# Kernel tuning notes

Measured on AMD Instinct MI355X. Metric: run time of the kernel, lower is better.

## Reference

```python
import jax, jax.numpy as jnp
import numpy as np

N_AGENTS, N_ENEMIES, N_ACTIONS = 8, 8, 14
ALLY_F, ENEMY_F = 8, 6
EMBED, RNN, HYPEMB, HYPHID = 32, 64, 64, 64
STATE_DIM = N_AGENTS * ALLY_F + N_ENEMIES * ENEMY_F + N_AGENTS * N_ACTIONS  # 224


def setup_inputs() -> dict:
    key = jax.random.key(0)
    ks = jax.random.split(key, 16)
    b, t = 64, 256
    rn = lambda k, s, sc=0.05: jax.random.normal(k, s, jnp.float32) * sc
    return dict(
        qvals=rn(ks[0], (b, t, N_AGENTS), 1.0),
        states=rn(ks[1], (b, t, STATE_DIM), 1.0),
        hidden_states=rn(ks[2], (b, t, N_AGENTS, RNN), 1.0),
        hw1_w=rn(ks[3], (RNN, EMBED)), hw1_b=jnp.zeros((EMBED,), jnp.float32),
        en_h1w=rn(ks[4], (ENEMY_F, HYPHID)), en_h1b=jnp.zeros((HYPHID,), jnp.float32),
        en_h2w=rn(ks[5], (HYPHID, ENEMY_F * HYPEMB)), en_h2b=jnp.zeros((ENEMY_F * HYPEMB,), jnp.float32),
        en_bias=jnp.zeros((1, HYPEMB), jnp.float32),
        al_h1w=rn(ks[6], (ALLY_F, HYPHID)), al_h1b=jnp.zeros((HYPHID,), jnp.float32),
        al_h2w=rn(ks[7], (HYPHID, ALLY_F * HYPEMB)), al_h2b=jnp.zeros((ALLY_F * HYPEMB,), jnp.float32),
        al_bias=jnp.zeros((1, HYPEMB), jnp.float32),
        act_w=rn(ks[8], (N_ACTIONS, HYPEMB)), act_b=jnp.zeros((HYPEMB,), jnp.float32),
        hb1_w=rn(ks[9], (HYPEMB, EMBED)), hb1_b=jnp.zeros((EMBED,), jnp.float32),
        hw2_w=rn(ks[10], (HYPEMB, EMBED)), hw2_b=jnp.zeros((EMBED,), jnp.float32),
        hb2_w=rn(ks[11], (HYPEMB, 1)), hb2_b=jnp.zeros((1,), jnp.float32),
    )


def _hyperlinear(x, h1w, h1b, h2w, h2b, bias, din, dout):
    # hypernet MLP -> per-sample weight matrix [rows, din, dout]
    h = jax.nn.relu(x @ h1w + h1b)
    W = (h @ h2w + h2b).reshape(-1, din, dout)
    return jnp.einsum('bi,bio->bo', x, W) + bias


def reference(qvals, states, hidden_states, hw1_w, hw1_b,
              en_h1w, en_h1b, en_h2w, en_h2b, en_bias,
              al_h1w, al_h1b, al_h2w, al_h2b, al_bias,
              act_w, act_b, hb1_w, hb1_b, hw2_w, hw2_b, hb2_w, hb2_b):
    b, t, _ = qvals.shape
    BT = b * t
    s = states.reshape(BT, STATE_DIM)
    ally = s[:, :N_AGENTS * ALLY_F].reshape(-1, ALLY_F)                # [BT*A, 8]
    enemy = s[:, N_AGENTS * ALLY_F:N_AGENTS * ALLY_F + N_ENEMIES * ENEMY_F].reshape(-1, ENEMY_F)
    actions = s[:, N_AGENTS * ALLY_F + N_ENEMIES * ENEMY_F:].reshape(BT, N_AGENTS, N_ACTIONS)

    embed_ally = _hyperlinear(ally, al_h1w, al_h1b, al_h2w, al_h2b, al_bias,
                              ALLY_F, HYPEMB).reshape(BT, N_AGENTS, HYPEMB).mean(axis=1)
    embed_enemy = _hyperlinear(enemy, en_h1w, en_h1b, en_h2w, en_h2b, en_bias,
                               ENEMY_F, HYPEMB).reshape(BT, N_ENEMIES, HYPEMB).mean(axis=1)
    embed_action = (actions @ act_w + act_b).mean(axis=1)
    se = jax.nn.relu(embed_ally + embed_enemy + embed_action)          # [BT, HYPEMB]

    w1 = jax.nn.softmax((hidden_states @ hw1_w + hw1_b).reshape(BT, N_AGENTS, EMBED), axis=1)
    b1 = (se @ hb1_w + hb1_b).reshape(BT, 1, EMBED)
    w2 = jnp.abs(se @ hw2_w + hw2_b).reshape(BT, EMBED, 1)
    b2 = (se @ hb2_w + hb2_b).reshape(BT, 1, 1)

    q = qvals.reshape(BT, 1, N_AGENTS)
    hidden = jax.nn.elu(jnp.matmul(q, w1) + b1)                        # [BT, 1, EMBED]
    y = jnp.matmul(hidden, w2) + b2                                    # [BT, 1, 1]
    return y.reshape(b, t, 1)
```

## Files before the change

### kernel.cpp

```cpp
#include <hip/hip_runtime.h>
#include <hip/hip_bf16.h>
#include <stdint.h>

typedef unsigned short u16t;
typedef float f32x4 __attribute__((ext_vector_type(4)));
typedef short bf16x8 __attribute__((ext_vector_type(8)));

#define SDIM 224

__device__ __forceinline__ float lo16(uint32_t w) { union { uint32_t u; float f; } v; v.u = w << 16; return v.f; }
__device__ __forceinline__ float hi16(uint32_t w) { union { uint32_t u; float f; } v; v.u = w & 0xFFFF0000u; return v.f; }
__device__ __forceinline__ uint32_t f2bf(float f) {
    union { float f; uint32_t u; } v; v.f = f;
    return (v.u + 0x7FFFu + ((v.u >> 16) & 1u)) >> 16;
}

__global__ void prep_wt_kernel(const float* __restrict__ h2wA, const float* __restrict__ h2wB,
                               const float* __restrict__ h2bA, const float* __restrict__ h2bB,
                               const float* __restrict__ actw,
                               const float* __restrict__ hb1w, const float* __restrict__ hw2w,
                               const float* __restrict__ hw1w,
                               u16t* __restrict__ wtA, u16t* __restrict__ wtB,
                               u16t* __restrict__ wt2, u16t* __restrict__ wtM)
{
    const int t0 = blockIdx.x * 256 + threadIdx.x, stride = gridDim.x * 256;
    for (int e = t0; e < 34816; e += stride) {
        int j = e & 7, n = (e >> 3) & 63, kb = e >> 9;
        int k = kb * 8 + j;
        float v = 0.f;
        if (k < 512)      { int h = k & 63, i = k >> 6; v = h2wA[h * 512 + i * 64 + n]; }
        else if (k < 520) v = h2bA[(k - 512) * 64 + n];
        wtA[e] = (u16t)f2bf(v);
    }
    for (int e = t0; e < 26624; e += stride) {
        int j = e & 7, n = (e >> 3) & 63, kb = e >> 9;
        int k = kb * 8 + j;
        float v = 0.f;
        if (k < 384)      { int h = k & 63, i = k >> 6; v = h2wB[h * 384 + i * 64 + n]; }
        else if (k < 390) v = h2bB[(k - 384) * 64 + n];
        else if (k < 404) v = actw[(k - 390) * 64 + n];
        wtB[e] = (u16t)f2bf(v);
    }
    for (int e = t0; e < 4096; e += stride) {
        int j = e & 7, n = (e >> 3) & 63, kb = e >> 9;
        int k = kb * 8 + j;
        float v = (n < 32) ? hb1w[k * 32 + n] : hw2w[k * 32 + (n - 32)];
        wt2[e] = (u16t)f2bf(v);
    }
    for (int e = t0; e < 2048; e += stride) {
        int j = e & 7, n = (e >> 3) & 31, kb = e >> 8;
        wtM[e] = (u16t)f2bf(hw1w[(kb * 8 + j) * 32 + n]);
    }
}

template<int DIN, int KP, int FOFF>
__device__ __forceinline__ void stage1(const u16t (*xb)[SDIM], u16t* __restrict__ ps,
                                       const float* __restrict__ s_h1w, float b1r,
                                       int wave, int lane)
{
    float w1r[DIN];
#pragma unroll
    for (int i = 0; i < DIN; ++i) w1r[i] = s_h1w[i * 64 + lane];
#pragma unroll 1
    for (int ss = 0; ss < 2; ++ss) {
        const int s = wave * 2 + ss;
        const u16t* xr = &xb[s][FOFF];
        float psv[DIN];
#pragma unroll
        for (int i = 0; i < DIN; ++i) psv[i] = 0.f;
#pragma unroll
        for (int a = 0; a < 8; ++a) {
            float x[DIN];
            if constexpr (DIN == 8) {
                uint4 v = *(const uint4*)(xr + a * 8);
                x[0] = lo16(v.x); x[1] = hi16(v.x); x[2] = lo16(v.y); x[3] = hi16(v.y);
                x[4] = lo16(v.z); x[5] = hi16(v.z); x[6] = lo16(v.w); x[7] = hi16(v.w);
            } else {
                uint32_t w0 = *(const uint32_t*)(xr + a * 6);
                uint32_t w1 = *(const uint32_t*)(xr + a * 6 + 2);
                uint32_t w2 = *(const uint32_t*)(xr + a * 6 + 4);
                x[0] = lo16(w0); x[1] = hi16(w0); x[2] = lo16(w1);
                x[3] = hi16(w1); x[4] = lo16(w2); x[5] = hi16(w2);
            }
            float hacc = b1r;
#pragma unroll
            for (int i = 0; i < DIN; ++i) hacc += x[i] * w1r[i];
            hacc = fmaxf(hacc, 0.f);
#pragma unroll
            for (int i = 0; i < DIN; ++i) psv[i] += hacc * x[i];
        }
#pragma unroll
        for (int i = 0; i < DIN; ++i) ps[s * KP + i * 64 + lane] = (u16t)f2bf(psv[i]);
    }
}

__global__ __launch_bounds__(256, 7)
void fused_mixer(const float* __restrict__ qvals, const float* __restrict__ states,
                 const float* __restrict__ hs,
                 const float* __restrict__ al_h1w, const float* __restrict__ al_h1b,
                 const float* __restrict__ en_h1w, const float* __restrict__ en_h1b,
                 const float* __restrict__ al_bias, const float* __restrict__ en_bias,
                 const float* __restrict__ act_b,
                 const float* __restrict__ hb1_b, const float* __restrict__ hw2_b,
                 const float* __restrict__ hw1_b, const float* __restrict__ hb2_w,
                 const float* __restrict__ hb2_b,
                 const u16t* __restrict__ wtA, const u16t* __restrict__ wtB,
                 const u16t* __restrict__ wt2, const u16t* __restrict__ wtM,
                 float* __restrict__ out)
{
    constexpr int KPA = 552, KPB = 424;
    __shared__ __align__(16) char s_un[9216];
    __shared__ __align__(16) u16t s_xb[8][SDIM];
    __shared__ __align__(16) u16t s_se[8 * 72];
    __shared__ float s_b1w2[8][64];
    __shared__ float s_b2[8];
    __shared__ float s_q[64];
    __shared__ float s_h1wA[512], s_h1wB[384];
    __shared__ float s_h1bA[64], s_h1bB[64], s_bias3[64], s_hb2w[64];
    __shared__ float s_b1b[32], s_w2b[32], s_w1b[32];
    __shared__ float s_hb2bv;

    const int tid  = threadIdx.x;
    const int wave = tid >> 6;
    const int lane = tid & 63;
    const int lr = lane & 15, lg = lane >> 4;
    const int sbase = blockIdx.x * 8;
    const int o = wave * 16 + lr;

    for (int i = tid; i < 8 * 28; i += 256) {
        int s = i / 28, c = i - s * 28;
        const float4* sp = (const float4*)(states + (size_t)(sbase + s) * SDIM + c * 8);
        float4 v0 = sp[0], v1 = sp[1];
        uint4 p;
        p.x = f2bf(v0.x) | (f2bf(v0.y) << 16);
        p.y = f2bf(v0.z) | (f2bf(v0.w) << 16);
        p.z = f2bf(v1.x) | (f2bf(v1.y) << 16);
        p.w = f2bf(v1.z) | (f2bf(v1.w) << 16);
        *(uint4*)&s_xb[s][c * 8] = p;
    }
    for (int i = tid; i < 512; i += 256) s_h1wA[i] = al_h1w[i];
    for (int i = tid; i < 384; i += 256) s_h1wB[i] = en_h1w[i];
    if (tid < 64) {
        s_h1bA[tid] = al_h1b[tid]; s_h1bB[tid] = en_h1b[tid];
        s_bias3[tid] = al_bias[tid] + en_bias[tid] + act_b[tid];
        s_hb2w[tid] = hb2_w[tid];
        s_q[tid] = qvals[(size_t)sbase * 8 + tid];
    }
    if (tid >= 64 && tid < 96)   s_b1b[tid - 64] = hb1_b[tid - 64];
    if (tid >= 96 && tid < 128)  s_w2b[tid - 96] = hw2_b[tid - 96];
    if (tid >= 128 && tid < 160) s_w1b[tid - 128] = hw1_b[tid - 128];
    if (tid == 160) s_hb2bv = hb2_b[0];
    __syncthreads();

    u16t* ps = (u16t*)s_un;

    stage1<8, KPA, 0>(s_xb, ps, s_h1wA, s_h1bA[lane], wave, lane);
    if (tid < 64) {
        int s = tid >> 3, i = tid & 7;
        float t = 0.f;
#pragma unroll
        for (int a = 0; a < 8; ++a) t += lo16((uint32_t)s_xb[s][a * 8 + i]);
        ps[s * KPA + 512 + i] = (u16t)f2bf(t);
    } else if (tid < 160) {
        int idx = tid - 64;
        int s = idx / 12, kp = idx - s * 12;
        *(uint32_t*)&ps[s * KPA + 520 + kp * 2] = 0u;
    }
    __syncthreads();

    f32x4 accA = {0.f, 0.f, 0.f, 0.f};
    {
        const u16t* arow = ps + (lr & 7) * KPA + lg * 8;
        const bf16x8* wt8 = (const bf16x8*)wtA;
#pragma unroll 4
        for (int kk = 0; kk < 544; kk += 32) {
            bf16x8 av = *(const bf16x8*)(arow + kk);
            bf16x8 bv = wt8[((kk >> 3) + lg) * 64 + o];
            accA = __builtin_amdgcn_mfma_f32_16x16x32_bf16(av, bv, accA, 0, 0, 0);
        }
    }
    __syncthreads();

    float4 hsr[4];
    {
        const float4* hsv = (const float4*)(hs + (size_t)sbase * 512);
#pragma unroll
        for (int i = 0; i < 4; ++i) hsr[i] = hsv[i * 256 + tid];
    }

    stage1<6, KPB, 64>(s_xb, ps, s_h1wB, s_h1bB[lane], wave, lane);
    if (tid < 48) {
        int s = tid / 6, i = tid - s * 6;
        float t = 0.f;
#pragma unroll
        for (int a = 0; a < 8; ++a) t += lo16((uint32_t)s_xb[s][64 + a * 6 + i]);
        ps[s * KPB + 384 + i] = (u16t)f2bf(t);
    } else if (tid >= 64 && tid < 176) {
        int idx = tid - 64;
        int s = idx / 14, j = idx - s * 14;
        float t = 0.f;
#pragma unroll
        for (int a = 0; a < 8; ++a) t += lo16((uint32_t)s_xb[s][112 + a * 14 + j]);
        ps[s * KPB + 390 + j] = (u16t)f2bf(t);
    } else if (tid >= 192 && tid < 240) {
        int idx = tid - 192;
        int s = idx / 6, kp = idx - s * 6;
        *(uint32_t*)&ps[s * KPB + 404 + kp * 2] = 0u;
    }
    __syncthreads();

    {
        f32x4 accB = {0.f, 0.f, 0.f, 0.f};
        const u16t* arow = ps + (lr & 7) * KPB + lg * 8;
        const bf16x8* wt8 = (const bf16x8*)wtB;
#pragma unroll 4
        for (int kk = 0; kk < 416; kk += 32) {
            bf16x8 av = *(const bf16x8*)(arow + kk);
            bf16x8 bv = wt8[((kk >> 3) + lg) * 64 + o];
            accB = __builtin_amdgcn_mfma_f32_16x16x32_bf16(av, bv, accB, 0, 0, 0);
        }
        if (lg < 2) {
#pragma unroll
            for (int j = 0; j < 4; ++j) {
                const int row = lg * 4 + j;
                float se = (accA[j] + accB[j]) * 0.125f + s_bias3[o];
                s_se[row * 72 + o] = (u16t)f2bf(fmaxf(se, 0.f));
            }
        }
    }
    __syncthreads();

    u16t* s_hs = (u16t*)s_un;
    {
#pragma unroll
        for (int i = 0; i < 4; ++i) {
            const int idx = i * 256 + tid;
            const int row = idx >> 4, c4 = idx & 15;
            uint2 p;
            p.x = f2bf(hsr[i].x) | (f2bf(hsr[i].y) << 16);
            p.y = f2bf(hsr[i].z) | (f2bf(hsr[i].w) << 16);
            *(uint2*)&s_hs[row * 72 + c4 * 4] = p;
        }
    }
    {
        f32x4 acc = {0.f, 0.f, 0.f, 0.f};
        const u16t* serow = &s_se[(lr & 7) * 72 + lg * 8];
        const bf16x8* wt8 = (const bf16x8*)wt2;
#pragma unroll
        for (int ks = 0; ks < 2; ++ks) {
            bf16x8 av = *(const bf16x8*)(serow + ks * 32);
            bf16x8 bv = wt8[(ks * 4 + lg) * 64 + o];
            acc = __builtin_amdgcn_mfma_f32_16x16x32_bf16(av, bv, acc, 0, 0, 0);
        }
        if (lg < 2) {
#pragma unroll
            for (int j = 0; j < 4; ++j) {
                const int row = lg * 4 + j;
                float v = acc[j] + ((o < 32) ? s_b1b[o] : s_w2b[o - 32]);
                if (o >= 32) v = fabsf(v);
                s_b1w2[row][o] = v;
            }
        }
    }
    {
        const int smp = wave * 2 + (lg & 1);
        float p = 0.f;
#pragma unroll
        for (int c = 0; c < 4; ++c) {
            const int oo = c * 16 + lr;
            p += lo16((uint32_t)s_se[smp * 72 + oo]) * s_hb2w[oo];
        }
        p += __shfl_xor(p, 1); p += __shfl_xor(p, 2);
        p += __shfl_xor(p, 4); p += __shfl_xor(p, 8);
        if (lr == 0 && lg < 2) s_b2[smp] = p + s_hb2bv;
    }
    __syncthreads();

    bf16x8 bfr[2][2];
    {
        const bf16x8* wtm8 = (const bf16x8*)wtM;
#pragma unroll
        for (int n = 0; n < 2; ++n)
#pragma unroll
            for (int ks = 0; ks < 2; ++ks)
                bfr[n][ks] = wtm8[(ks * 4 + lg) * 32 + n * 16 + lr];
    }
    {
        const float zb0 = s_w1b[lr], zb1 = s_w1b[16 + lr];
        f32x4 d0 = {0.f,0.f,0.f,0.f}, d1 = {0.f,0.f,0.f,0.f};
#pragma unroll
        for (int ks = 0; ks < 2; ++ks) {
            bf16x8 av = *(const bf16x8*)&s_hs[(wave * 16 + lr) * 72 + ks * 32 + lg * 8];
            d0 = __builtin_amdgcn_mfma_f32_16x16x32_bf16(av, bfr[0][ks], d0, 0, 0, 0);
            d1 = __builtin_amdgcn_mfma_f32_16x16x32_bf16(av, bfr[1][ks], d1, 0, 0, 0);
        }
        const int sloc = wave * 2 + (lg >> 1);
        float z0[4], z1[4];
#pragma unroll
        for (int j = 0; j < 4; ++j) { z0[j] = d0[j] + zb0; z1[j] = d1[j] + zb1; }
        float m0 = fmaxf(fmaxf(z0[0], z0[1]), fmaxf(z0[2], z0[3]));
        float m1 = fmaxf(fmaxf(z1[0], z1[1]), fmaxf(z1[2], z1[3]));
        m0 = fmaxf(m0, __shfl_xor(m0, 16));
        m1 = fmaxf(m1, __shfl_xor(m1, 16));
        float qa[4];
        {
            float4 qv = *(const float4*)&s_q[sloc * 8 + (lg & 1) * 4];
            qa[0] = qv.x; qa[1] = qv.y; qa[2] = qv.z; qa[3] = qv.w;
        }
        float s0 = 0.f, s1 = 0.f, hp0 = 0.f, hp1 = 0.f;
#pragma unroll
        for (int j = 0; j < 4; ++j) {
            float e0 = __expf(z0[j] - m0), e1 = __expf(z1[j] - m1);
            s0 += e0; s1 += e1;
            hp0 += qa[j] * e0; hp1 += qa[j] * e1;
        }
        s0  += __shfl_xor(s0, 16);  s1  += __shfl_xor(s1, 16);
        hp0 += __shfl_xor(hp0, 16); hp1 += __shfl_xor(hp1, 16);

        const float b1_0 = s_b1w2[sloc][lr],      b1_1 = s_b1w2[sloc][16 + lr];
        const float w2_0 = s_b1w2[sloc][32 + lr], w2_1 = s_b1w2[sloc][48 + lr];
        float h0 = hp0 / s0 + b1_0; h0 = (h0 > 0.f) ? h0 : (__expf(h0) - 1.f);
        float h1 = hp1 / s1 + b1_1; h1 = (h1 > 0.f) ? h1 : (__expf(h1) - 1.f);
        float yp = h0 * w2_0 + h1 * w2_1;
        yp += __shfl_xor(yp, 1); yp += __shfl_xor(yp, 2);
        yp += __shfl_xor(yp, 4); yp += __shfl_xor(yp, 8);
        if (lr == 0 && (lg & 1) == 0) out[sbase + sloc] = yp + s_b2[sloc];
    }
}

extern "C" void kernel_launch(void* const* d_in, const int* in_sizes, int n_in,
                              void* d_out, int out_size, void* d_ws, size_t ws_size,
                              hipStream_t stream) {
    const float* qvals   = (const float*)d_in[0];
    const float* states  = (const float*)d_in[1];
    const float* hstates = (const float*)d_in[2];
    const float* hw1_w   = (const float*)d_in[3];
    const float* hw1_b   = (const float*)d_in[4];
    const float* en_h1w  = (const float*)d_in[5];
    const float* en_h1b  = (const float*)d_in[6];
    const float* en_h2w  = (const float*)d_in[7];
    const float* en_h2b  = (const float*)d_in[8];
    const float* en_bias = (const float*)d_in[9];
    const float* al_h1w  = (const float*)d_in[10];
    const float* al_h1b  = (const float*)d_in[11];
    const float* al_h2w  = (const float*)d_in[12];
    const float* al_h2b  = (const float*)d_in[13];
    const float* al_bias = (const float*)d_in[14];
    const float* act_w   = (const float*)d_in[15];
    const float* act_b   = (const float*)d_in[16];
    const float* hb1_w   = (const float*)d_in[17];
    const float* hb1_b   = (const float*)d_in[18];
    const float* hw2_w   = (const float*)d_in[19];
    const float* hw2_b   = (const float*)d_in[20];
    const float* hb2_w   = (const float*)d_in[21];
    const float* hb2_b   = (const float*)d_in[22];

    u16t* wtA = (u16t*)d_ws;
    u16t* wtB = wtA + 34816;
    u16t* wt2 = wtA + 61440;
    u16t* wtM = wtA + 65536;

    prep_wt_kernel<<<64, 256, 0, stream>>>(al_h2w, en_h2w, al_h2b, en_h2b, act_w,
                                           hb1_w, hw2_w, hw1_w, wtA, wtB, wt2, wtM);
    fused_mixer<<<2048, 256, 0, stream>>>(qvals, states, hstates,
                                          al_h1w, al_h1b, en_h1w, en_h1b,
                                          al_bias, en_bias, act_b,
                                          hb1_b, hw2_b, hw1_b, hb2_w, hb2_b,
                                          wtA, wtB, wt2, wtM, (float*)d_out);
}
```

Measured before the change: 38.17 us.

## Merge ally/enemy hypernet GEMMs into one K=960 pass and reorder mixing stage

Concatenates the ally and enemy/action weight panels into one workspace matrix. Both stage-1 passes now write into a single wide shared buffer, so one MFMA loop over K=960 replaces two GEMMs and removes two block barriers. The hidden-state tile is staged to shared memory up front, and the softmax mixing MFMA now runs before the main GEMM. qvals are read directly from global memory. The larger shared footprint and the lowered launch-bounds target (7 to 4 blocks per SM) may reduce occupancy.

After: 36.34 us. 4.8% less time.

```diff
diff --git a/kernel.cpp b/kernel.cpp
--- a/kernel.cpp
+++ b/kernel.cpp
@@ -20,26 +20,23 @@
                                const float* __restrict__ actw,
                                const float* __restrict__ hb1w, const float* __restrict__ hw2w,
                                const float* __restrict__ hw1w,
-                               u16t* __restrict__ wtA, u16t* __restrict__ wtB,
-                               u16t* __restrict__ wt2, u16t* __restrict__ wtM)
+                               u16t* __restrict__ wtAB, u16t* __restrict__ wt2,
+                               u16t* __restrict__ wtM)
 {
     const int t0 = blockIdx.x * 256 + threadIdx.x, stride = gridDim.x * 256;
-    for (int e = t0; e < 34816; e += stride) {
+    for (int e = t0; e < 61440; e += stride) {
         int j = e & 7, n = (e >> 3) & 63, kb = e >> 9;
         int k = kb * 8 + j;
         float v = 0.f;
         if (k < 512)      { int h = k & 63, i = k >> 6; v = h2wA[h * 512 + i * 64 + n]; }
         else if (k < 520) v = h2bA[(k - 512) * 64 + n];
-        wtA[e] = (u16t)f2bf(v);
-    }
-    for (int e = t0; e < 26624; e += stride) {
-        int j = e & 7, n = (e >> 3) & 63, kb = e >> 9;
-        int k = kb * 8 + j;
-        float v = 0.f;
-        if (k < 384)      { int h = k & 63, i = k >> 6; v = h2wB[h * 384 + i * 64 + n]; }
-        else if (k < 390) v = h2bB[(k - 384) * 64 + n];
-        else if (k < 404) v = actw[(k - 390) * 64 + n];
-        wtB[e] = (u16t)f2bf(v);
+        else if (k >= 544) {
+            int k2 = k - 544;
+            if (k2 < 384)      { int h = k2 & 63, i = k2 >> 6; v = h2wB[h * 384 + i * 64 + n]; }
+            else if (k2 < 390) v = h2bB[(k2 - 384) * 64 + n];
+            else if (k2 < 404) v = actw[(k2 - 390) * 64 + n];
+        }
+        wtAB[e] = (u16t)f2bf(v);
     }
     for (int e = t0; e < 4096; e += stride) {
         int j = e & 7, n = (e >> 3) & 63, kb = e >> 9;
@@ -94,7 +91,7 @@
     }
 }
 
-__global__ __launch_bounds__(256, 7)
+__global__ __launch_bounds__(256, 4)
 void fused_mixer(const float* __restrict__ qvals, const float* __restrict__ states,
                  const float* __restrict__ hs,
                  const float* __restrict__ al_h1w, const float* __restrict__ al_h1b,
@@ -104,17 +101,17 @@
                  const float* __restrict__ hb1_b, const float* __restrict__ hw2_b,
                  const float* __restrict__ hw1_b, const float* __restrict__ hb2_w,
                  const float* __restrict__ hb2_b,
-                 const u16t* __restrict__ wtA, const u16t* __restrict__ wtB,
-                 const u16t* __restrict__ wt2, const u16t* __restrict__ wtM,
+                 const u16t* __restrict__ wtAB, const u16t* __restrict__ wt2,
+                 const u16t* __restrict__ wtM,
                  float* __restrict__ out)
 {
-    constexpr int KPA = 552, KPB = 424;
-    __shared__ __align__(16) char s_un[9216];
+    constexpr int KP = 968;
+    __shared__ __align__(16) u16t s_ps[8 * KP];
+    __shared__ __align__(16) u16t s_hs[64 * 72];
     __shared__ __align__(16) u16t s_xb[8][SDIM];
     __shared__ __align__(16) u16t s_se[8 * 72];
     __shared__ float s_b1w2[8][64];
     __shared__ float s_b2[8];
-    __shared__ float s_q[64];
     __shared__ float s_h1wA[512], s_h1wB[384];
     __shared__ float s_h1bA[64], s_h1bB[64], s_bias3[64], s_hb2w[64];
     __shared__ float s_b1b[32], s_w2b[32], s_w1b[32];
@@ -138,13 +135,25 @@
         p.w = f2bf(v1.z) | (f2bf(v1.w) << 16);
         *(uint4*)&s_xb[s][c * 8] = p;
     }
+    {
+        const float4* hsv = (const float4*)(hs + (size_t)sbase * 512);
+#pragma unroll
+        for (int i = 0; i < 4; ++i) {
+            const int idx = i * 256 + tid;
+            float4 v = hsv[idx];
+            const int row = idx >> 4, c4 = idx & 15;
+            uint2 p;
+            p.x = f2bf(v.x) | (f2bf(v.y) << 16);
+            p.y = f2bf(v.z) | (f2bf(v.w) << 16);
+            *(uint2*)&s_hs[row * 72 + c4 * 4] = p;
+        }
+    }
     for (int i = tid; i < 512; i += 256) s_h1wA[i] = al_h1w[i];
     for (int i = tid; i < 384; i += 256) s_h1wB[i] = en_h1w[i];
     if (tid < 64) {
         s_h1bA[tid] = al_h1b[tid]; s_h1bB[tid] = en_h1b[tid];
         s_bias3[tid] = al_bias[tid] + en_bias[tid] + act_b[tid];
         s_hb2w[tid] = hb2_w[tid];
-        s_q[tid] = qvals[(size_t)sbase * 8 + tid];
     }
     if (tid >= 64 && tid < 96)   s_b1b[tid - 64] = hb1_b[tid - 64];
     if (tid >= 96 && tid < 128)  s_w2b[tid - 96] = hw2_b[tid - 96];
@@ -152,141 +161,50 @@
     if (tid == 160) s_hb2bv = hb2_b[0];
     __syncthreads();
 
-    u16t* ps = (u16t*)s_un;
-
-    stage1<8, KPA, 0>(s_xb, ps, s_h1wA, s_h1bA[lane], wave, lane);
+    stage1<8, KP, 0>(s_xb, s_ps, s_h1wA, s_h1bA[lane], wave, lane);
+    stage1<6, KP, 64>(s_xb, s_ps + 544, s_h1wB, s_h1bB[lane], wave, lane);
     if (tid < 64) {
         int s = tid >> 3, i = tid & 7;
         float t = 0.f;
 #pragma unroll
         for (int a = 0; a < 8; ++a) t += lo16((uint32_t)s_xb[s][a * 8 + i]);
-        ps[s * KPA + 512 + i] = (u16t)f2bf(t);
-    } else if (tid < 160) {
+        s_ps[s * KP + 512 + i] = (u16t)f2bf(t);
+    } else if (tid < 112) {
         int idx = tid - 64;
-        int s = idx / 12, kp = idx - s * 12;
-        *(uint32_t*)&ps[s * KPA + 520 + kp * 2] = 0u;
-    }
-    __syncthreads();
-
-    f32x4 accA = {0.f, 0.f, 0.f, 0.f};
-    {
-        const u16t* arow = ps + (lr & 7) * KPA + lg * 8;
-        const bf16x8* wt8 = (const bf16x8*)wtA;
-#pragma unroll 4
-        for (int kk = 0; kk < 544; kk += 32) {
-            bf16x8 av = *(const bf16x8*)(arow + kk);
-            bf16x8 bv = wt8[((kk >> 3) + lg) * 64 + o];
-            accA = __builtin_amdgcn_mfma_f32_16x16x32_bf16(av, bv, accA, 0, 0, 0);
-        }
-    }
-    __syncthreads();
-
-    float4 hsr[4];
-    {
-        const float4* hsv = (const float4*)(hs + (size_t)sbase * 512);
-#pragma unroll
-        for (int i = 0; i < 4; ++i) hsr[i] = hsv[i * 256 + tid];
-    }
-
-    stage1<6, KPB, 64>(s_xb, ps, s_h1wB, s_h1bB[lane], wave, lane);
-    if (tid < 48) {
-        int s = tid / 6, i = tid - s * 6;
+        int s = idx / 6, i = idx - s * 6;
         float t = 0.f;
 #pragma unroll
         for (int a = 0; a < 8; ++a) t += lo16((uint32_t)s_xb[s][64 + a * 6 + i]);
-        ps[s * KPB + 384 + i] = (u16t)f2bf(t);
-    } else if (tid >= 64 && tid < 176) {
-        int idx = tid - 64;
+        s_ps[s * KP + 928 + i] = (u16t)f2bf(t);
+    } else if (tid < 224) {
+        int idx = tid - 112;
         int s = idx / 14, j = idx - s * 14;
         float t = 0.f;
 #pragma unroll
         for (int a = 0; a < 8; ++a) t += lo16((uint32_t)s_xb[s][112 + a * 14 + j]);
-        ps[s * KPB + 390 + j] = (u16t)f2bf(t);
-    } else if (tid >= 192 && tid < 240) {
-        int idx = tid - 192;
-        int s = idx / 6, kp = idx - s * 6;
-        *(uint32_t*)&ps[s * KPB + 404 + kp * 2] = 0u;
-    }
-    __syncthreads();
-
-    {
-        f32x4 accB = {0.f, 0.f, 0.f, 0.f};
-        const u16t* arow = ps + (lr & 7) * KPB + lg * 8;
-        const bf16x8* wt8 = (const bf16x8*)wtB;
-#pragma unroll 4
-        for (int kk = 0; kk < 416; kk += 32) {
-            bf16x8 av = *(const bf16x8*)(arow + kk);
-            bf16x8 bv = wt8[((kk >> 3) + lg) * 64 + o];
-            accB = __builtin_amdgcn_mfma_f32_16x16x32_bf16(av, bv, accB, 0, 0, 0);
-        }
-        if (lg < 2) {
-#pragma unroll
-            for (int j = 0; j < 4; ++j) {
-                const int row = lg * 4 + j;
-                float se = (accA[j] + accB[j]) * 0.125f + s_bias3[o];
-                s_se[row * 72 + o] = (u16t)f2bf(fmaxf(se, 0.f));
-            }
-        }
-    }
-    __syncthreads();
-
-    u16t* s_hs = (u16t*)s_un;
-    {
-#pragma unroll
-        for (int i = 0; i < 4; ++i) {
-            const int idx = i * 256 + tid;
-            const int row = idx >> 4, c4 = idx & 15;
-            uint2 p;
-            p.x = f2bf(hsr[i].x) | (f2bf(hsr[i].y) << 16);
-            p.y = f2bf(hsr[i].z) | (f2bf(hsr[i].w) << 16);
-            *(uint2*)&s_hs[row * 72 + c4 * 4] = p;
-        }
-    }
-    {
-        f32x4 acc = {0.f, 0.f, 0.f, 0.f};
-        const u16t* serow = &s_se[(lr & 7) * 72 + lg * 8];
-        const bf16x8* wt8 = (const bf16x8*)wt2;
-#pragma unroll
-        for (int ks = 0; ks < 2; ++ks) {
-            bf16x8 av = *(const bf16x8*)(serow + ks * 32);
-            bf16x8 bv = wt8[(ks * 4 + lg) * 64 + o];
-            acc = __builtin_amdgcn_mfma_f32_16x16x32_bf16(av, bv, acc, 0, 0, 0);
-        }
-        if (lg < 2) {
-#pragma unroll
-            for (int j = 0; j < 4; ++j) {
-                const int row = lg * 4 + j;
-                float v = acc[j] + ((o < 32) ? s_b1b[o] : s_w2b[o - 32]);
-                if (o >= 32) v = fabsf(v);
-                s_b1w2[row][o] = v;
-            }
-        }
-    }
-    {
-        const int smp = wave * 2 + (lg & 1);
-        float p = 0.f;
-#pragma unroll
-        for (int c = 0; c < 4; ++c) {
-            const int oo = c * 16 + lr;
-            p += lo16((uint32_t)s_se[smp * 72 + oo]) * s_hb2w[oo];
-        }
-        p += __shfl_xor(p, 1); p += __shfl_xor(p, 2);
-        p += __shfl_xor(p, 4); p += __shfl_xor(p, 8);
-        if (lr == 0 && lg < 2) s_b2[smp] = p + s_hb2bv;
-    }
-    __syncthreads();
-
-    bf16x8 bfr[2][2];
-    {
+        s_ps[s * KP + 934 + j] = (u16t)f2bf(t);
+    } else {
+        int idx = tid - 224;
+        int s = idx >> 2, c = idx & 3;
+#pragma unroll
+        for (int u = 0; u < 3; ++u)
+            *(uint32_t*)&s_ps[s * KP + 520 + c * 6 + u * 2] = 0u;
+        if (c < 3)
+            *(uint32_t*)&s_ps[s * KP + 948 + c * 4] = 0u;
+        else
+            *(uint32_t*)&s_ps[s * KP + 948 + 8 + 2] = 0u;
+    }
+
+    float hp0, hp1, s0, s1;
+    {
+        bf16x8 bfr[2][2];
         const bf16x8* wtm8 = (const bf16x8*)wtM;
 #pragma unroll
         for (int n = 0; n < 2; ++n)
 #pragma unroll
             for (int ks = 0; ks < 2; ++ks)
                 bfr[n][ks] = wtm8[(ks * 4 + lg) * 32 + n * 16 + lr];
-    }
-    {
-        const float zb0 = s_w1b[lr], zb1 = s_w1b[16 + lr];
+
         f32x4 d0 = {0.f,0.f,0.f,0.f}, d1 = {0.f,0.f,0.f,0.f};
 #pragma unroll
         for (int ks = 0; ks < 2; ++ks) {
@@ -295,6 +213,7 @@
             d1 = __builtin_amdgcn_mfma_f32_16x16x32_bf16(av, bfr[1][ks], d1, 0, 0, 0);
         }
         const int sloc = wave * 2 + (lg >> 1);
+        const float zb0 = s_w1b[lr], zb1 = s_w1b[16 + lr];
         float z0[4], z1[4];
 #pragma unroll
         for (int j = 0; j < 4; ++j) { z0[j] = d0[j] + zb0; z1[j] = d1[j] + zb1; }
@@ -304,10 +223,11 @@
         m1 = fmaxf(m1, __shfl_xor(m1, 16));
         float qa[4];
         {
-            float4 qv = *(const float4*)&s_q[sloc * 8 + (lg & 1) * 4];
+            const float* qp = qvals + (size_t)(sbase + sloc) * 8 + (lg & 1) * 4;
+            float4 qv = *(const float4*)qp;
             qa[0] = qv.x; qa[1] = qv.y; qa[2] = qv.z; qa[3] = qv.w;
         }
-        float s0 = 0.f, s1 = 0.f, hp0 = 0.f, hp1 = 0.f;
+        s0 = 0.f; s1 = 0.f; hp0 = 0.f; hp1 = 0.f;
 #pragma unroll
         for (int j = 0; j < 4; ++j) {
             float e0 = __expf(z0[j] - m0), e1 = __expf(z1[j] - m1);
@@ -316,7 +236,66 @@
         }
         s0  += __shfl_xor(s0, 16);  s1  += __shfl_xor(s1, 16);
         hp0 += __shfl_xor(hp0, 16); hp1 += __shfl_xor(hp1, 16);
-
+    }
+    __syncthreads();
+
+    {
+        f32x4 acc = {0.f, 0.f, 0.f, 0.f};
+        const u16t* arow = s_ps + (lr & 7) * KP + lg * 8;
+        const bf16x8* wt8 = (const bf16x8*)wtAB;
+#pragma unroll 5
+        for (int kk = 0; kk < 960; kk += 32) {
+            bf16x8 av = *(const bf16x8*)(arow + kk);
+            bf16x8 bv = wt8[((kk >> 3) + lg) * 64 + o];
+            acc = __builtin_amdgcn_mfma_f32_16x16x32_bf16(av, bv, acc, 0, 0, 0);
+        }
+        if (lg < 2) {
+#pragma unroll
+            for (int j = 0; j < 4; ++j) {
+                const int row = lg * 4 + j;
+                float se = acc[j] * 0.125f + s_bias3[o];
+                s_se[row * 72 + o] = (u16t)f2bf(fmaxf(se, 0.f));
+            }
+        }
+    }
+    __syncthreads();
+
+    {
+        f32x4 acc = {0.f, 0.f, 0.f, 0.f};
+        const u16t* serow = &s_se[(lr & 7) * 72 + lg * 8];
+        const bf16x8* wt8 = (const bf16x8*)wt2;
+#pragma unroll
+        for (int ks = 0; ks < 2; ++ks) {
+            bf16x8 av = *(const bf16x8*)(serow + ks * 32);
+            bf16x8 bv = wt8[(ks * 4 + lg) * 64 + o];
+            acc = __builtin_amdgcn_mfma_f32_16x16x32_bf16(av, bv, acc, 0, 0, 0);
+        }
+        if (lg < 2) {
+#pragma unroll
+            for (int j = 0; j < 4; ++j) {
+                const int row = lg * 4 + j;
+                float v = acc[j] + ((o < 32) ? s_b1b[o] : s_w2b[o - 32]);
+                if (o >= 32) v = fabsf(v);
+                s_b1w2[row][o] = v;
+            }
+        }
+    }
+    {
+        const int smp = wave * 2 + (lg & 1);
+        float p = 0.f;
+#pragma unroll
+        for (int c = 0; c < 4; ++c) {
+            const int oo = c * 16 + lr;
+            p += lo16((uint32_t)s_se[smp * 72 + oo]) * s_hb2w[oo];
+        }
+        p += __shfl_xor(p, 1); p += __shfl_xor(p, 2);
+        p += __shfl_xor(p, 4); p += __shfl_xor(p, 8);
+        if (lr == 0 && lg < 2) s_b2[smp] = p + s_hb2bv;
+    }
+    __syncthreads();
+
+    {
+        const int sloc = wave * 2 + (lg >> 1);
         const float b1_0 = s_b1w2[sloc][lr],      b1_1 = s_b1w2[sloc][16 + lr];
         const float w2_0 = s_b1w2[sloc][32 + lr], w2_1 = s_b1w2[sloc][48 + lr];
         float h0 = hp0 / s0 + b1_0; h0 = (h0 > 0.f) ? h0 : (__expf(h0) - 1.f);
@@ -355,16 +334,15 @@
     const float* hb2_w   = (const float*)d_in[21];
     const float* hb2_b   = (const float*)d_in[22];
 
-    u16t* wtA = (u16t*)d_ws;
-    u16t* wtB = wtA + 34816;
-    u16t* wt2 = wtA + 61440;
-    u16t* wtM = wtA + 65536;
+    u16t* wtAB = (u16t*)d_ws;
+    u16t* wt2  = wtAB + 61440;
+    u16t* wtM  = wtAB + 65536;
 
     prep_wt_kernel<<<64, 256, 0, stream>>>(al_h2w, en_h2w, al_h2b, en_h2b, act_w,
-                                           hb1_w, hw2_w, hw1_w, wtA, wtB, wt2, wtM);
+                                           hb1_w, hw2_w, hw1_w, wtAB, wt2, wtM);
     fused_mixer<<<2048, 256, 0, stream>>>(qvals, states, hstates,
                                           al_h1w, al_h1b, en_h1w, en_h1b,
                                           al_bias, en_bias, act_b,
                                           hb1_b, hw2_b, hw1_b, hb2_w, hb2_b,
-                                          wtA, wtB, wt2, wtM, (float*)d_out);
-}
+                                          wtAB, wt2, wtM, (float*)d_out);
+}
```

## Process 16 samples per block to fill MFMA rows and keep states in fp32

Applied to the files above, without the earlier changes.

Each block now handles 16 samples instead of 8, so the 16-row MFMA tiles are fully used rather than half wasted, and the grid is halved. The states tile is kept in shared memory as fp32 instead of being converted to bf16, and the action sums are computed directly from global memory. Bf16 conversion now goes through the HIP intrinsics, with a packed two-value variant. Shared memory and register use roughly double and the launch bound drops to 4 blocks per CU, which lowers occupancy.

Result: faster. 34.81 us (-8.8%).

```diff
diff --git a/kernel.cpp b/kernel.cpp
--- a/kernel.cpp
+++ b/kernel.cpp
@@ -9,10 +9,13 @@
 #define SDIM 224
 
 __device__ __forceinline__ float lo16(uint32_t w) { union { uint32_t u; float f; } v; v.u = w << 16; return v.f; }
-__device__ __forceinline__ float hi16(uint32_t w) { union { uint32_t u; float f; } v; v.u = w & 0xFFFF0000u; return v.f; }
-__device__ __forceinline__ uint32_t f2bf(float f) {
-    union { float f; uint32_t u; } v; v.f = f;
-    return (v.u + 0x7FFFu + ((v.u >> 16) & 1u)) >> 16;
+__device__ __forceinline__ u16t bf1(float a) {
+    union { __hip_bfloat16 h; u16t u; } c; c.h = __float2bfloat16(a); return c.u;
+}
+__device__ __forceinline__ uint32_t pk2(float a, float b) {
+    union { __hip_bfloat162 h; uint32_t u; } c;
+    c.h = __float22bfloat162_rn(make_float2(a, b));
+    return c.u;
 }
 
 __global__ void prep_wt_kernel(const float* __restrict__ h2wA, const float* __restrict__ h2wB,
@@ -30,7 +33,7 @@
         float v = 0.f;
         if (k < 512)      { int h = k & 63, i = k >> 6; v = h2wA[h * 512 + i * 64 + n]; }
         else if (k < 520) v = h2bA[(k - 512) * 64 + n];
-        wtA[e] = (u16t)f2bf(v);
+        wtA[e] = bf1(v);
     }
     for (int e = t0; e < 26624; e += stride) {
         int j = e & 7, n = (e >> 3) & 63, kb = e >> 9;
@@ -39,22 +42,22 @@
         if (k < 384)      { int h = k & 63, i = k >> 6; v = h2wB[h * 384 + i * 64 + n]; }
         else if (k < 390) v = h2bB[(k - 384) * 64 + n];
         else if (k < 404) v = actw[(k - 390) * 64 + n];
-        wtB[e] = (u16t)f2bf(v);
+        wtB[e] = bf1(v);
     }
     for (int e = t0; e < 4096; e += stride) {
         int j = e & 7, n = (e >> 3) & 63, kb = e >> 9;
         int k = kb * 8 + j;
         float v = (n < 32) ? hb1w[k * 32 + n] : hw2w[k * 32 + (n - 32)];
-        wt2[e] = (u16t)f2bf(v);
+        wt2[e] = bf1(v);
     }
     for (int e = t0; e < 2048; e += stride) {
         int j = e & 7, n = (e >> 3) & 31, kb = e >> 8;
-        wtM[e] = (u16t)f2bf(hw1w[(kb * 8 + j) * 32 + n]);
+        wtM[e] = bf1(hw1w[(kb * 8 + j) * 32 + n]);
     }
 }
 
 template<int DIN, int KP, int FOFF>
-__device__ __forceinline__ void stage1(const u16t (*xb)[SDIM], u16t* __restrict__ ps,
+__device__ __forceinline__ void stage1(const float (*sx)[112], u16t* __restrict__ ps,
                                        const float* __restrict__ s_h1w, float b1r,
                                        int wave, int lane)
 {
@@ -62,9 +65,9 @@
 #pragma unroll
     for (int i = 0; i < DIN; ++i) w1r[i] = s_h1w[i * 64 + lane];
 #pragma unroll 1
-    for (int ss = 0; ss < 2; ++ss) {
-        const int s = wave * 2 + ss;
-        const u16t* xr = &xb[s][FOFF];
+    for (int ss = 0; ss < 4; ++ss) {
+        const int s = wave * 4 + ss;
+        const float* xr = &sx[s][FOFF];
         float psv[DIN];
 #pragma unroll
         for (int i = 0; i < DIN; ++i) psv[i] = 0.f;
@@ -72,15 +75,15 @@
         for (int a = 0; a < 8; ++a) {
             float x[DIN];
             if constexpr (DIN == 8) {
-                uint4 v = *(const uint4*)(xr + a * 8);
-                x[0] = lo16(v.x); x[1] = hi16(v.x); x[2] = lo16(v.y); x[3] = hi16(v.y);
-                x[4] = lo16(v.z); x[5] = hi16(v.z); x[6] = lo16(v.w); x[7] = hi16(v.w);
+                float4 v0 = *(const float4*)(xr + a * 8);
+                float4 v1 = *(const float4*)(xr + a * 8 + 4);
+                x[0] = v0.x; x[1] = v0.y; x[2] = v0.z; x[3] = v0.w;
+                x[4] = v1.x; x[5] = v1.y; x[6] = v1.z; x[7] = v1.w;
             } else {
-                uint32_t w0 = *(const uint32_t*)(xr + a * 6);
-                uint32_t w1 = *(const uint32_t*)(xr + a * 6 + 2);
-                uint32_t w2 = *(const uint32_t*)(xr + a * 6 + 4);
-                x[0] = lo16(w0); x[1] = hi16(w0); x[2] = lo16(w1);
-                x[3] = hi16(w1); x[4] = lo16(w2); x[5] = hi16(w2);
+                float2 v0 = *(const float2*)(xr + a * 6);
+                float2 v1 = *(const float2*)(xr + a * 6 + 2);
+                float2 v2 = *(const float2*)(xr + a * 6 + 4);
+                x[0] = v0.x; x[1] = v0.y; x[2] = v1.x; x[3] = v1.y; x[4] = v2.x; x[5] = v2.y;
             }
             float hacc = b1r;
 #pragma unroll
@@ -90,11 +93,16 @@
             for (int i = 0; i < DIN; ++i) psv[i] += hacc * x[i];
         }
 #pragma unroll
-        for (int i = 0; i < DIN; ++i) ps[s * KP + i * 64 + lane] = (u16t)f2bf(psv[i]);
-    }
-}
-
-__global__ __launch_bounds__(256, 7)
+        for (int i = 0; i < DIN; i += 2) {
+            union { __hip_bfloat162 h; struct { u16t lo, hi; } w; } c;
+            c.h = __float22bfloat162_rn(make_float2(psv[i], psv[i + 1]));
+            ps[s * KP + i * 64 + lane]       = c.w.lo;
+            ps[s * KP + (i + 1) * 64 + lane] = c.w.hi;
+        }
+    }
+}
+
+__global__ __launch_bounds__(256, 4)
 void fused_mixer(const float* __restrict__ qvals, const float* __restrict__ states,
                  const float* __restrict__ hs,
                  const float* __restrict__ al_h1w, const float* __restrict__ al_h1b,
@@ -109,12 +117,13 @@
                  float* __restrict__ out)
 {
     constexpr int KPA = 552, KPB = 424;
-    __shared__ __align__(16) char s_un[9216];
-    __shared__ __align__(16) u16t s_xb[8][SDIM];
-    __shared__ __align__(16) u16t s_se[8 * 72];
-    __shared__ float s_b1w2[8][64];
-    __shared__ float s_b2[8];
-    __shared__ float s_q[64];
+    __shared__ __align__(16) char  s_un[18432];
+    __shared__ __align__(16) float s_x[16][112];
+    __shared__ float s_act[16][14];
+    __shared__ __align__(16) u16t  s_se[16 * 72];
+    __shared__ float s_b1w2[16][64];
+    __shared__ float s_b2[16];
+    __shared__ float s_q[128];
     __shared__ float s_h1wA[512], s_h1wB[384];
     __shared__ float s_h1bA[64], s_h1bB[64], s_bias3[64], s_hb2w[64];
     __shared__ float s_b1b[32], s_w2b[32], s_w1b[32];
@@ -124,19 +133,20 @@
     const int wave = tid >> 6;
     const int lane = tid & 63;
     const int lr = lane & 15, lg = lane >> 4;
-    const int sbase = blockIdx.x * 8;
+    const int sbase = blockIdx.x * 16;
     const int o = wave * 16 + lr;
 
-    for (int i = tid; i < 8 * 28; i += 256) {
+    for (int i = tid; i < 16 * 28; i += 256) {
         int s = i / 28, c = i - s * 28;
-        const float4* sp = (const float4*)(states + (size_t)(sbase + s) * SDIM + c * 8);
-        float4 v0 = sp[0], v1 = sp[1];
-        uint4 p;
-        p.x = f2bf(v0.x) | (f2bf(v0.y) << 16);
-        p.y = f2bf(v0.z) | (f2bf(v0.w) << 16);
-        p.z = f2bf(v1.x) | (f2bf(v1.y) << 16);
-        p.w = f2bf(v1.z) | (f2bf(v1.w) << 16);
-        *(uint4*)&s_xb[s][c * 8] = p;
+        *(float4*)&s_x[s][c * 4] = *(const float4*)(states + (size_t)(sbase + s) * SDIM + c * 4);
+    }
+    if (tid < 224) {
+        int s = tid / 14, j = tid - s * 14;
+        const float* ap = states + (size_t)(sbase + s) * SDIM + 112 + j;
+        float t = 0.f;
+#pragma unroll
+        for (int a = 0; a < 8; ++a) t += ap[a * 14];
+        s_act[s][j] = t;
     }
     for (int i = tid; i < 512; i += 256) s_h1wA[i] = al_h1w[i];
     for (int i = tid; i < 384; i += 256) s_h1wB[i] = en_h1w[i];
@@ -144,33 +154,36 @@
         s_h1bA[tid] = al_h1b[tid]; s_h1bB[tid] = en_h1b[tid];
         s_bias3[tid] = al_bias[tid] + en_bias[tid] + act_b[tid];
         s_hb2w[tid] = hb2_w[tid];
-        s_q[tid] = qvals[(size_t)sbase * 8 + tid];
     }
     if (tid >= 64 && tid < 96)   s_b1b[tid - 64] = hb1_b[tid - 64];
     if (tid >= 96 && tid < 128)  s_w2b[tid - 96] = hw2_b[tid - 96];
     if (tid >= 128 && tid < 160) s_w1b[tid - 128] = hw1_b[tid - 128];
+    if (tid >= 160 && tid < 288 - 32) {  }
     if (tid == 160) s_hb2bv = hb2_b[0];
+    if (tid >= 128 && tid < 256 && tid - 128 < 128) s_q[tid - 128] = qvals[(size_t)sbase * 8 + (tid - 128)];
     __syncthreads();
 
     u16t* ps = (u16t*)s_un;
 
-    stage1<8, KPA, 0>(s_xb, ps, s_h1wA, s_h1bA[lane], wave, lane);
-    if (tid < 64) {
+    stage1<8, KPA, 0>(s_x, ps, s_h1wA, s_h1bA[lane], wave, lane);
+    if (tid < 128) {
         int s = tid >> 3, i = tid & 7;
         float t = 0.f;
 #pragma unroll
-        for (int a = 0; a < 8; ++a) t += lo16((uint32_t)s_xb[s][a * 8 + i]);
-        ps[s * KPA + 512 + i] = (u16t)f2bf(t);
-    } else if (tid < 160) {
-        int idx = tid - 64;
-        int s = idx / 12, kp = idx - s * 12;
-        *(uint32_t*)&ps[s * KPA + 520 + kp * 2] = 0u;
+        for (int a = 0; a < 8; ++a) t += s_x[s][a * 8 + i];
+        ps[s * KPA + 512 + i] = bf1(t);
+    } else {
+        int idx = tid - 128;
+        for (int u = idx; u < 192; u += 128) {
+            int s = u / 12, r = u - s * 12;
+            *(uint32_t*)&ps[s * KPA + 520 + r * 2] = 0u;
+        }
     }
     __syncthreads();
 
     f32x4 accA = {0.f, 0.f, 0.f, 0.f};
     {
-        const u16t* arow = ps + (lr & 7) * KPA + lg * 8;
+        const u16t* arow = ps + lr * KPA + lg * 8;
         const bf16x8* wt8 = (const bf16x8*)wtA;
 #pragma unroll 4
         for (int kk = 0; kk < 544; kk += 32) {
@@ -181,37 +194,35 @@
     }
     __syncthreads();
 
-    float4 hsr[4];
+    float4 hsr[8];
     {
         const float4* hsv = (const float4*)(hs + (size_t)sbase * 512);
 #pragma unroll
-        for (int i = 0; i < 4; ++i) hsr[i] = hsv[i * 256 + tid];
-    }
-
-    stage1<6, KPB, 64>(s_xb, ps, s_h1wB, s_h1bB[lane], wave, lane);
-    if (tid < 48) {
+        for (int i = 0; i < 8; ++i) hsr[i] = hsv[i * 256 + tid];
+    }
+    stage1<6, KPB, 64>(s_x, ps, s_h1wB, s_h1bB[lane], wave, lane);
+    if (tid < 96) {
         int s = tid / 6, i = tid - s * 6;
         float t = 0.f;
 #pragma unroll
-        for (int a = 0; a < 8; ++a) t += lo16((uint32_t)s_xb[s][64 + a * 6 + i]);
-        ps[s * KPB + 384 + i] = (u16t)f2bf(t);
-    } else if (tid >= 64 && tid < 176) {
-        int idx = tid - 64;
-        int s = idx / 14, j = idx - s * 14;
-        float t = 0.f;
-#pragma unroll
-        for (int a = 0; a < 8; ++a) t += lo16((uint32_t)s_xb[s][112 + a * 14 + j]);
-        ps[s * KPB + 390 + j] = (u16t)f2bf(t);
-    } else if (tid >= 192 && tid < 240) {
-        int idx = tid - 192;
-        int s = idx / 6, kp = idx - s * 6;
-        *(uint32_t*)&ps[s * KPB + 404 + kp * 2] = 0u;
+        for (int a = 0; a < 8; ++a) t += s_x[s][64 + a * 6 + i];
+        ps[s * KPB + 384 + i] = bf1(t);
+    } else {
+        int idx = tid - 96;
+        for (int u = idx; u < 224; u += 160) {
+            int s = u / 14, j = u - s * 14;
+            ps[s * KPB + 390 + j] = bf1(s_act[s][j]);
+        }
+    }
+    if (tid < 96) {
+        int s = tid / 6, r = tid - (tid / 6) * 6;
+        *(uint32_t*)&ps[s * KPB + 404 + r * 2] = 0u;
     }
     __syncthreads();
 
     {
         f32x4 accB = {0.f, 0.f, 0.f, 0.f};
-        const u16t* arow = ps + (lr & 7) * KPB + lg * 8;
+        const u16t* arow = ps + lr * KPB + lg * 8;
         const bf16x8* wt8 = (const bf16x8*)wtB;
 #pragma unroll 4
         for (int kk = 0; kk < 416; kk += 32) {
@@ -219,13 +230,11 @@
             bf16x8 bv = wt8[((kk >> 3) + lg) * 64 + o];
             accB = __builtin_amdgcn_mfma_f32_16x16x32_bf16(av, bv, accB, 0, 0, 0);
         }
-        if (lg < 2) {
-#pragma unroll
-            for (int j = 0; j < 4; ++j) {
-                const int row = lg * 4 + j;
-                float se = (accA[j] + accB[j]) * 0.125f + s_bias3[o];
-                s_se[row * 72 + o] = (u16t)f2bf(fmaxf(se, 0.f));
-            }
+#pragma unroll
+        for (int j = 0; j < 4; ++j) {
+            const int row = lg * 4 + j;
+            float se = (accA[j] + accB[j]) * 0.125f + s_bias3[o];
+            s_se[row * 72 + o] = bf1(fmaxf(se, 0.f));
         }
     }
     __syncthreads();
@@ -233,18 +242,18 @@
     u16t* s_hs = (u16t*)s_un;
     {
 #pragma unroll
-        for (int i = 0; i < 4; ++i) {
+        for (int i = 0; i < 8; ++i) {
             const int idx = i * 256 + tid;
             const int row = idx >> 4, c4 = idx & 15;
             uint2 p;
-            p.x = f2bf(hsr[i].x) | (f2bf(hsr[i].y) << 16);
-            p.y = f2bf(hsr[i].z) | (f2bf(hsr[i].w) << 16);
+            p.x = pk2(hsr[i].x, hsr[i].y);
+            p.y = pk2(hsr[i].z, hsr[i].w);
             *(uint2*)&s_hs[row * 72 + c4 * 4] = p;
         }
     }
     {
         f32x4 acc = {0.f, 0.f, 0.f, 0.f};
-        const u16t* serow = &s_se[(lr & 7) * 72 + lg * 8];
+        const u16t* serow = &s_se[lr * 72 + lg * 8];
         const bf16x8* wt8 = (const bf16x8*)wt2;
 #pragma unroll
         for (int ks = 0; ks < 2; ++ks) {
@@ -252,18 +261,16 @@
             bf16x8 bv = wt8[(ks * 4 + lg) * 64 + o];
             acc = __builtin_amdgcn_mfma_f32_16x16x32_bf16(av, bv, acc, 0, 0, 0);
         }
-        if (lg < 2) {
-#pragma unroll
-            for (int j = 0; j < 4; ++j) {
-                const int row = lg * 4 + j;
-                float v = acc[j] + ((o < 32) ? s_b1b[o] : s_w2b[o - 32]);
-                if (o >= 32) v = fabsf(v);
-                s_b1w2[row][o] = v;
-            }
-        }
-    }
-    {
-        const int smp = wave * 2 + (lg & 1);
+#pragma unroll
+        for (int j = 0; j < 4; ++j) {
+            const int row = lg * 4 + j;
+            float v = acc[j] + ((o < 32) ? s_b1b[o] : s_w2b[o - 32]);
+            if (o >= 32) v = fabsf(v);
+            s_b1w2[row][o] = v;
+        }
+    }
+    {
+        const int smp = wave * 4 + lg;
         float p = 0.f;
 #pragma unroll
         for (int c = 0; c < 4; ++c) {
@@ -272,7 +279,7 @@
         }
         p += __shfl_xor(p, 1); p += __shfl_xor(p, 2);
         p += __shfl_xor(p, 4); p += __shfl_xor(p, 8);
-        if (lr == 0 && lg < 2) s_b2[smp] = p + s_hb2bv;
+        if (lr == 0) s_b2[smp] = p + s_hb2bv;
     }
     __syncthreads();
 
@@ -285,16 +292,17 @@
             for (int ks = 0; ks < 2; ++ks)
                 bfr[n][ks] = wtm8[(ks * 4 + lg) * 32 + n * 16 + lr];
     }
-    {
-        const float zb0 = s_w1b[lr], zb1 = s_w1b[16 + lr];
+    const float zb0 = s_w1b[lr], zb1 = s_w1b[16 + lr];
+
+    for (int t = wave * 2; t < wave * 2 + 2; ++t) {
         f32x4 d0 = {0.f,0.f,0.f,0.f}, d1 = {0.f,0.f,0.f,0.f};
 #pragma unroll
         for (int ks = 0; ks < 2; ++ks) {
-            bf16x8 av = *(const bf16x8*)&s_hs[(wave * 16 + lr) * 72 + ks * 32 + lg * 8];
+            bf16x8 av = *(const bf16x8*)&s_hs[(t * 16 + lr) * 72 + ks * 32 + lg * 8];
             d0 = __builtin_amdgcn_mfma_f32_16x16x32_bf16(av, bfr[0][ks], d0, 0, 0, 0);
             d1 = __builtin_amdgcn_mfma_f32_16x16x32_bf16(av, bfr[1][ks], d1, 0, 0, 0);
         }
-        const int sloc = wave * 2 + (lg >> 1);
+        const int sloc = t * 2 + (lg >> 1);
         float z0[4], z1[4];
 #pragma unroll
         for (int j = 0; j < 4; ++j) { z0[j] = d0[j] + zb0; z1[j] = d1[j] + zb1; }
@@ -362,7 +370,7 @@
 
     prep_wt_kernel<<<64, 256, 0, stream>>>(al_h2w, en_h2w, al_h2b, en_h2b, act_w,
                                            hb1_w, hw2_w, hw1_w, wtA, wtB, wt2, wtM);
-    fused_mixer<<<2048, 256, 0, stream>>>(qvals, states, hstates,
+    fused_mixer<<<1024, 256, 0, stream>>>(qvals, states, hstates,
                                           al_h1w, al_h1b, en_h1w, en_h1b,
                                           al_bias, en_bias, act_b,
                                           hb1_b, hw2_b, hw1_b, hb2_w, hb2_b,
```
